# Optimization experiments

Hardware: AMD Instinct MI355X
Metric: run time of the kernel (lower is better)

## Reference

```python
import jax, jax.numpy as jnp
import numpy as np

B, N, E = 16, 64, 512
C_IMG = 512
H1, H2, H3 = 256, 128, 64
U, R = 8, 8
BBC = 9
EH1, EH2 = 64, 64
BBOX_POS_MAX = 1024.0
EPS = 1e-5


def setup_inputs():
    key = jax.random.key(0)
    ks = jax.random.split(key, 24)
    f = lambda i, shape, s=0.05: jax.random.normal(ks[i], shape, jnp.float32) * s
    return {
        'roi_features': f(0, (B, N, C_IMG), 1.0),
        'batch_bboxes': jax.random.uniform(ks[1], (B, N, 4)) * BBOX_POS_MAX,
        'batch_directions': jax.random.uniform(ks[2], (B, N, 4)),
        'batch_priorities': jax.random.uniform(ks[3], (B, N)),
        'w1': f(4, (C_IMG, H1)), 'b1': f(5, (H1,)),
        'bn1_g': jnp.ones((H1,)), 'bn1_b': jnp.zeros((H1,)),
        'bn1_m': jnp.zeros((H1,)), 'bn1_v': jnp.ones((H1,)),
        'w2': f(6, (H1, H2)), 'b2': f(7, (H2,)),
        'bn2_g': jnp.ones((H2,)), 'bn2_b': jnp.zeros((H2,)),
        'bn2_m': jnp.zeros((H2,)), 'bn2_v': jnp.ones((H2,)),
        'w3': f(8, (H2, H3)), 'b3': f(9, (H3,)),
        'wn': f(10, (H3, U)), 'bn_c': f(11, (U,)),
        'we1': f(12, (2 * BBC, EH1)), 'be1': f(13, (EH1,)),
        'we2': f(14, (EH1, EH2)), 'be2': f(15, (EH2,)),
        'wei': f(16, (EH2, R)), 'bei': f(17, (R,)),
        'edge_index': jax.random.randint(ks[18], (B, 2, E), 0, N, dtype=jnp.int32),
    }


def _bn(x, g, b, m, v):
    # BatchNorm1d in eval mode (running stats)
    return (x - m) * jax.lax.rsqrt(v + EPS) * g + b


def _build_see(edge_index):
    # Padded neighbor table replacing edge_index2dict:
    # see[b,n,0] = n, then srcs of edges with dst==n, in original edge order.
    src = edge_index[:, 0, :]                                   # [B,E]
    dst = edge_index[:, 1, :]                                   # [B,E]
    eq = dst[:, :, None] == dst[:, None, :]                     # [B,E,E]
    lower = jnp.tril(jnp.ones((E, E), bool), -1)
    pos = jnp.sum(eq & lower, axis=-1) + 1                      # rank within dst group, +1 for self slot
    see = jnp.zeros((B, N, N), jnp.int32).at[:, :, 0].set(jnp.arange(N, dtype=jnp.int32))
    b_idx = jnp.arange(B)[:, None]
    see = see.at[b_idx, dst, pos].set(src, mode='drop')
    deg = jnp.zeros((B, N), jnp.int32).at[b_idx, dst].add(1)
    count = jnp.minimum(deg + 1, N)
    mask = (jnp.arange(N)[None, None, :] < count[:, :, None]).astype(jnp.float32)  # [B,N,N]
    return see, mask


def _forward(roi_features, batch_bboxes, batch_directions, batch_priorities,
             w1, b1, bn1_g, bn1_b, bn1_m, bn1_v,
             w2, b2, bn2_g, bn2_b, bn2_m, bn2_v,
             w3, b3, wn, bn_c,
             we1, be1, we2, be2, wei, bei, edge_index):
    see, mask = _build_see(edge_index)
    # --- node branch (node_predictor + node_concept_interpreter) ---
    x = roi_features.reshape(B * N, C_IMG)
    x = jax.nn.relu(_bn(x @ w1 + b1, bn1_g, bn1_b, bn1_m, bn1_v))
    x = jax.nn.relu(_bn(x @ w2 + b2, bn2_g, bn2_b, bn2_m, bn2_v))
    x = jax.nn.relu(x @ w3 + b3)
    node_c = jax.nn.sigmoid(x @ wn + bn_c).reshape(B, N, U)
    # get_nlm_unary_concepts: gather per-node neighborhood into dense [B,N,N,U]
    gu = jax.vmap(lambda u, s: u[s])(node_c, see)               # [B,N,N,U]
    node_concepts = (gu * mask[..., None]).reshape(B * N, N, U)
    # --- edge branch ---
    attr = jnp.concatenate([batch_bboxes / BBOX_POS_MAX, batch_directions,
                            batch_priorities[..., None]], axis=-1)  # [B,N,BBC]
    pair = jnp.concatenate([
        jnp.broadcast_to(attr[:, :, None, :], (B, N, N, BBC)),
        jnp.broadcast_to(attr[:, None, :, :], (B, N, N, BBC))], axis=-1).reshape(-1, 2 * BBC)
    e = jax.nn.relu(pair @ we1 + be1)
    e = jax.nn.relu(e @ we2 + be2)
    rel = jax.nn.sigmoid(e @ wei + bei).reshape(B, N, N, R)
    # get_nlm_binary_concepts: rel[b, see[b,n,i], see[b,n,j]] with zero padding
    def per_b(r, s, m):
        g = r[s[:, :, None], s[:, None, :]]                     # [N,N,N,R]
        return g * (m[:, :, None, None] * m[:, None, :, None])
    edge_concepts = jax.vmap(per_b)(rel, see, mask).reshape(B * N, N, N, R)
    return node_concepts, edge_concepts


def reference(roi_features, batch_bboxes, batch_directions, batch_priorities,
              w1, b1, bn1_g, bn1_b, bn1_m, bn1_v,
              w2, b2, bn2_g, bn2_b, bn2_m, bn2_v,
              w3, b3, wn, bn_c,
              we1, be1, we2, be2, wei, bei, edge_index):
    return _forward(roi_features, batch_bboxes, batch_directions, batch_priorities,
                    w1, b1, bn1_g, bn1_b, bn1_m, bn1_v,
                    w2, b2, bn2_g, bn2_b, bn2_m, bn2_v,
                    w3, b3, wn, bn_c,
                    we1, be1, we2, be2, wei, bei, edge_index)
```

## Files before the change

kernel.cpp:

```cpp
#include <hip/hip_runtime.h>
#include <math.h>

#define BB    16
#define NN    64
#define EE    512
#define CIMG  512
#define H1D   256
#define H2D   128
#define H3D   64
#define UD    8
#define RD    8
#define BBCD  9
#define EH1D  64
#define EH2D  64
#define EPSF  1e-5f

typedef float nfloat4 __attribute__((ext_vector_type(4)));

__global__ __launch_bounds__(256) void fused1_kernel(
    const int* __restrict__ edge_index,
    const float* __restrict__ bboxes,
    const float* __restrict__ dirs,
    const float* __restrict__ prios,
    const float* __restrict__ we1,
    const float* __restrict__ be1,
    int* __restrict__ see, int* __restrict__ cnt,
    float* __restrict__ P, float* __restrict__ Q,
    const float* __restrict__ roi,
    const float* __restrict__ w1, const float* __restrict__ b1,
    const float* __restrict__ g1, const float* __restrict__ bt1,
    const float* __restrict__ m1, const float* __restrict__ v1,
    const float* __restrict__ w2, const float* __restrict__ b2,
    const float* __restrict__ g2, const float* __restrict__ bt2,
    const float* __restrict__ m2, const float* __restrict__ v2,
    const float* __restrict__ w3, const float* __restrict__ b3,
    const float* __restrict__ wn, const float* __restrict__ bnc,
    float* __restrict__ node_c,
    float* __restrict__ out_edge)
{
    __shared__ union {
        struct {
            int src[EE];
            int dst[EE];
            int see[NN * NN];
            float attr[NN][BBCD];
        } p;
        struct {
            float part[4096];
            float h1[4][H1D];
            float h2[4][H2D];
            float h3[4][H3D];
        } n;
    } sm;

    const int t = threadIdx.x;

    if (blockIdx.x >= BB + 256) {
        const int id = blockIdx.x - (BB + 256);
        nfloat4* dst = (nfloat4*)(out_edge + (size_t)id * NN * NN * RD);
        const nfloat4 z = {0.f, 0.f, 0.f, 0.f};
        #pragma unroll
        for (int it = 0; it < 16; ++it) {
            int task = it * 256 + t;
            __builtin_nontemporal_store(z, dst + task * 2);
            __builtin_nontemporal_store(z, dst + task * 2 + 1);
        }
        return;
    }

    if (blockIdx.x < BB) {
        const int b = blockIdx.x;
        const int* ei = edge_index + b * 2 * EE;
        for (int e = t; e < EE; e += 256) {
            sm.p.src[e] = ei[e];
            sm.p.dst[e] = ei[EE + e];
        }
        for (int x = t; x < NN * NN; x += 256)
            sm.p.see[x] = ((x & (NN - 1)) == 0) ? (x >> 6) : 0;
        if (t < NN) {
            const float* bbp = bboxes + (b * NN + t) * 4;
            const float* ddp = dirs + (b * NN + t) * 4;
            sm.p.attr[t][0] = bbp[0] * (1.0f / 1024.0f);
            sm.p.attr[t][1] = bbp[1] * (1.0f / 1024.0f);
            sm.p.attr[t][2] = bbp[2] * (1.0f / 1024.0f);
            sm.p.attr[t][3] = bbp[3] * (1.0f / 1024.0f);
            sm.p.attr[t][4] = ddp[0];
            sm.p.attr[t][5] = ddp[1];
            sm.p.attr[t][6] = ddp[2];
            sm.p.attr[t][7] = ddp[3];
            sm.p.attr[t][8] = prios[b * NN + t];
        }
        __syncthreads();

        if (t < NN) {
            int pos = 0;
            #pragma unroll 8
            for (int e = 0; e < EE; ++e) {
                if (sm.p.dst[e] == t) {
                    ++pos;
                    if (pos < NN) sm.p.see[t * NN + pos] = sm.p.src[e];
                }
            }
            int c = pos + 1;
            cnt[b * NN + t] = (c < NN) ? c : NN;
        }
        __syncthreads();

        {
            int4* dst4 = (int4*)(see + b * NN * NN);
            const int4* src4 = (const int4*)sm.p.see;
            for (int x = t; x < (NN * NN) / 4; x += 256) dst4[x] = src4[x];
        }

        for (int x = t; x < NN * EH1D; x += 256) {
            int n = x >> 6, o = x & 63;
            float p = 0.f;
            float q = be1[o];
            #pragma unroll
            for (int c = 0; c < BBCD; ++c) {
                float a = sm.p.attr[n][c];
                p = fmaf(a, we1[c * EH1D + o], p);
                q = fmaf(a, we1[(BBCD + c) * EH1D + o], q);
            }
            P[(b * NN + n) * EH1D + o] = p;
            Q[(b * NN + n) * EH1D + o] = q;
        }
        return;
    }

    const int row0 = (blockIdx.x - BB) * 4;
    float* part = sm.n.part;

    {
        const int og = t & 63, kg = t >> 6;
        const float4* w1v = (const float4*)w1;
        const float4* roiv = (const float4*)(roi + (size_t)row0 * CIMG);
        float acc[4][4];
        #pragma unroll
        for (int r = 0; r < 4; ++r)
            #pragma unroll
            for (int c = 0; c < 4; ++c) acc[r][c] = 0.f;

        for (int cq = 0; cq < 32; ++cq) {
            const int c4 = kg * 32 + cq;
            float x[4][4], w[4][4];
            #pragma unroll
            for (int r = 0; r < 4; ++r) {
                float4 v = roiv[r * 128 + c4];
                x[r][0] = v.x; x[r][1] = v.y; x[r][2] = v.z; x[r][3] = v.w;
            }
            #pragma unroll
            for (int q = 0; q < 4; ++q) {
                float4 v = w1v[(size_t)(c4 * 4 + q) * 64 + og];
                w[q][0] = v.x; w[q][1] = v.y; w[q][2] = v.z; w[q][3] = v.w;
            }
            #pragma unroll
            for (int r = 0; r < 4; ++r)
                #pragma unroll
                for (int q = 0; q < 4; ++q)
                    #pragma unroll
                    for (int c = 0; c < 4; ++c)
                        acc[r][c] = fmaf(x[r][q], w[q][c], acc[r][c]);
        }
        #pragma unroll
        for (int r = 0; r < 4; ++r) {
            float4 v = {acc[r][0], acc[r][1], acc[r][2], acc[r][3]};
            *(float4*)(part + (kg * 4 + r) * 256 + og * 4) = v;
        }
    }
    __syncthreads();
    {
        const int o = t;
        const float bias = b1[o];
        const float scale = rsqrtf(v1[o] + EPSF) * g1[o];
        const float beta = bt1[o];
        const float mu = m1[o];
        #pragma unroll
        for (int r = 0; r < 4; ++r) {
            float s = part[(0 * 4 + r) * 256 + o] + part[(1 * 4 + r) * 256 + o]
                    + part[(2 * 4 + r) * 256 + o] + part[(3 * 4 + r) * 256 + o];
            sm.n.h1[r][o] = fmaxf(0.f, (s + bias - mu) * scale + beta);
        }
    }
    __syncthreads();

    {
        const int og = t & 31, kg = t >> 5;
        const float4* w2v = (const float4*)w2;
        float acc[4][4];
        #pragma unroll
        for (int r = 0; r < 4; ++r)
            #pragma unroll
            for (int c = 0; c < 4; ++c) acc[r][c] = 0.f;

        #pragma unroll
        for (int cq = 0; cq < 8; ++cq) {
            const int c4 = kg * 8 + cq;
            float x[4][4], w[4][4];
            #pragma unroll
            for (int r = 0; r < 4; ++r) {
                float4 v = *(const float4*)&sm.n.h1[r][c4 * 4];
                x[r][0] = v.x; x[r][1] = v.y; x[r][2] = v.z; x[r][3] = v.w;
            }
            #pragma unroll
            for (int q = 0; q < 4; ++q) {
                float4 v = w2v[(size_t)(c4 * 4 + q) * 32 + og];
                w[q][0] = v.x; w[q][1] = v.y; w[q][2] = v.z; w[q][3] = v.w;
            }
            #pragma unroll
            for (int r = 0; r < 4; ++r)
                #pragma unroll
                for (int q = 0; q < 4; ++q)
                    #pragma unroll
                    for (int c = 0; c < 4; ++c)
                        acc[r][c] = fmaf(x[r][q], w[q][c], acc[r][c]);
        }
        #pragma unroll
        for (int r = 0; r < 4; ++r) {
            float4 v = {acc[r][0], acc[r][1], acc[r][2], acc[r][3]};
            *(float4*)(part + (kg * 4 + r) * 128 + og * 4) = v;
        }
    }
    __syncthreads();
    {
        const int o = t & 127;
        const int rp = t >> 7;
        const float bias = b2[o];
        const float scale = rsqrtf(v2[o] + EPSF) * g2[o];
        const float beta = bt2[o];
        const float mu = m2[o];
        #pragma unroll
        for (int rr = 0; rr < 2; ++rr) {
            const int r = rp + rr * 2;
            float s = 0.f;
            #pragma unroll
            for (int kg = 0; kg < 8; ++kg) s += part[(kg * 4 + r) * 128 + o];
            sm.n.h2[r][o] = fmaxf(0.f, (s + bias - mu) * scale + beta);
        }
    }
    __syncthreads();

    {
        const int og = t & 15, kg = t >> 4;
        const float4* w3v = (const float4*)w3;
        float acc[4][4];
        #pragma unroll
        for (int r = 0; r < 4; ++r)
            #pragma unroll
            for (int c = 0; c < 4; ++c) acc[r][c] = 0.f;

        #pragma unroll
        for (int cq = 0; cq < 2; ++cq) {
            const int c4 = kg * 2 + cq;
            float x[4][4], w[4][4];
            #pragma unroll
            for (int r = 0; r < 4; ++r) {
                float4 v = *(const float4*)&sm.n.h2[r][c4 * 4];
                x[r][0] = v.x; x[r][1] = v.y; x[r][2] = v.z; x[r][3] = v.w;
            }
            #pragma unroll
            for (int q = 0; q < 4; ++q) {
                float4 v = w3v[(size_t)(c4 * 4 + q) * 16 + og];
                w[q][0] = v.x; w[q][1] = v.y; w[q][2] = v.z; w[q][3] = v.w;
            }
            #pragma unroll
            for (int r = 0; r < 4; ++r)
                #pragma unroll
                for (int q = 0; q < 4; ++q)
                    #pragma unroll
                    for (int c = 0; c < 4; ++c)
                        acc[r][c] = fmaf(x[r][q], w[q][c], acc[r][c]);
        }
        #pragma unroll
        for (int r = 0; r < 4; ++r) {
            float4 v = {acc[r][0], acc[r][1], acc[r][2], acc[r][3]};
            *(float4*)(part + (kg * 4 + r) * 64 + og * 4) = v;
        }
    }
    __syncthreads();
    {
        const int o = t & 63;
        const int r = t >> 6;
        float s = b3[o];
        #pragma unroll
        for (int kg = 0; kg < 16; ++kg) s += part[(kg * 4 + r) * 64 + o];
        sm.n.h3[r][o] = fmaxf(0.f, s);
    }
    __syncthreads();

    if (t < 32) {
        const int o = t & 7, r = t >> 3;
        float a = bnc[o];
        #pragma unroll 8
        for (int c = 0; c < H3D; ++c) a = fmaf(sm.n.h3[r][c], wn[c * UD + o], a);
        node_c[(size_t)(row0 + r) * UD + o] = 1.f / (1.f + expf(-a));
    }
}

__global__ __launch_bounds__(256) void edge_mlp_kernel(
    const float* __restrict__ P, const float* __restrict__ Q,
    const float* __restrict__ we2, const float* __restrict__ be2,
    const float* __restrict__ wei, const float* __restrict__ bei,
    float* __restrict__ rel)
{
    __shared__ float e1_s[NN * 68];
    __shared__ float qw_s[NN * EH1D];
    __shared__ float wei_s[EH2D * RD];
    __shared__ float Pi_s[EH1D];
    __shared__ float be2_s[EH2D];
    __shared__ float bei_s[RD];

    const int t = threadIdx.x;
    const int b = blockIdx.x >> 6;
    const int i = blockIdx.x & 63;

    {
        const float4* Qb4 = (const float4*)(Q + (size_t)b * NN * EH1D);
        float4* qw4 = (float4*)qw_s;
        #pragma unroll
        for (int x = 0; x < 4; ++x) qw4[x * 256 + t] = Qb4[x * 256 + t];
        if (t < EH1D) Pi_s[t] = P[(size_t)(b * NN + i) * EH1D + t];
        if (t < 128) ((float4*)wei_s)[t] = ((const float4*)wei)[t];
        if (t < EH2D) be2_s[t] = be2[t];
        if (t < RD) bei_s[t] = bei[t];
    }
    __syncthreads();

    {
        const int j = t & 63, cg = t >> 6;
        const float4* qrow = (const float4*)(qw_s + j * EH1D);
        const float4* prow = (const float4*)Pi_s;
        #pragma unroll
        for (int q = 0; q < 4; ++q) {
            int c4 = cg * 4 + q;
            float4 qv = qrow[c4];
            float4 pv = prow[c4];
            float4 ev;
            ev.x = fmaxf(0.f, qv.x + pv.x);
            ev.y = fmaxf(0.f, qv.y + pv.y);
            ev.z = fmaxf(0.f, qv.z + pv.z);
            ev.w = fmaxf(0.f, qv.w + pv.w);
            *(float4*)(e1_s + j * 68 + c4 * 4) = ev;
        }
    }
    __syncthreads();

    {
        const float4* w4 = (const float4*)we2;
        float4* qw4 = (float4*)qw_s;
        #pragma unroll
        for (int x = 0; x < 4; ++x) qw4[x * 256 + t] = w4[x * 256 + t];
    }
    __syncthreads();

    const int tx = t & 15, ty = t >> 4;
    const int o0 = tx * 4, j0 = ty * 4;
    float acc[4][4];
    #pragma unroll
    for (int r = 0; r < 4; ++r)
        #pragma unroll
        for (int o = 0; o < 4; ++o) acc[r][o] = 0.f;

    #pragma unroll 4
    for (int cg = 0; cg < 16; ++cg) {
        float ev[4][4];
        #pragma unroll
        for (int r = 0; r < 4; ++r) {
            float4 v = *(const float4*)(e1_s + (j0 + r) * 68 + cg * 4);
            ev[r][0] = v.x; ev[r][1] = v.y; ev[r][2] = v.z; ev[r][3] = v.w;
        }
        #pragma unroll
        for (int q = 0; q < 4; ++q) {
            float4 wv = *(const float4*)(qw_s + (cg * 4 + q) * EH1D + o0);
            #pragma unroll
            for (int r = 0; r < 4; ++r) {
                acc[r][0] = fmaf(ev[r][q], wv.x, acc[r][0]);
                acc[r][1] = fmaf(ev[r][q], wv.y, acc[r][1]);
                acc[r][2] = fmaf(ev[r][q], wv.z, acc[r][2]);
                acc[r][3] = fmaf(ev[r][q], wv.w, acc[r][3]);
            }
        }
    }

    {
        float4 bv = *(const float4*)(be2_s + o0);
        #pragma unroll
        for (int r = 0; r < 4; ++r) {
            float4 v;
            v.x = fmaxf(0.f, acc[r][0] + bv.x);
            v.y = fmaxf(0.f, acc[r][1] + bv.y);
            v.z = fmaxf(0.f, acc[r][2] + bv.z);
            v.w = fmaxf(0.f, acc[r][3] + bv.w);
            *(float4*)(e1_s + (j0 + r) * 68 + o0) = v;
        }
    }
    __syncthreads();

    {
        const int j = t >> 2;
        const int r0 = (t & 3) * 2;
        float a0 = bei_s[r0], a1 = bei_s[r0 + 1];
        const float* e2row = e1_s + j * 68;
        #pragma unroll
        for (int og = 0; og < 16; ++og) {
            float4 e2v = *(const float4*)(e2row + og * 4);
            float2 w0 = *(const float2*)(wei_s + (og * 4 + 0) * RD + r0);
            float2 w1 = *(const float2*)(wei_s + (og * 4 + 1) * RD + r0);
            float2 w2 = *(const float2*)(wei_s + (og * 4 + 2) * RD + r0);
            float2 w3 = *(const float2*)(wei_s + (og * 4 + 3) * RD + r0);
            a0 = fmaf(e2v.x, w0.x, a0); a1 = fmaf(e2v.x, w0.y, a1);
            a0 = fmaf(e2v.y, w1.x, a0); a1 = fmaf(e2v.y, w1.y, a1);
            a0 = fmaf(e2v.z, w2.x, a0); a1 = fmaf(e2v.z, w2.y, a1);
            a0 = fmaf(e2v.w, w3.x, a0); a1 = fmaf(e2v.w, w3.y, a1);
        }
        float2 o;
        o.x = 1.f / (1.f + expf(-a0));
        o.y = 1.f / (1.f + expf(-a1));
        *(float2*)(rel + ((size_t)(b * NN + i) * NN + j) * RD + r0) = o;
    }
}

__global__ __launch_bounds__(256) void gather_kernel(
    const int* __restrict__ see, const int* __restrict__ cnt,
    const float* __restrict__ node_c, const float* __restrict__ rel,
    float* __restrict__ out_node, float* __restrict__ out_edge)
{
    __shared__ int s_s[NN];

    const int t = threadIdx.x;
    const int bi = blockIdx.x;
    const int b = bi >> 6;
    const int c = cnt[bi];

    if (t < NN) s_s[t] = see[bi * NN + t];
    __syncthreads();

    if (t < NN) {
        const float m = (t < c) ? 1.f : 0.f;
        const float4* src = (const float4*)(node_c + (size_t)(b * NN + s_s[t]) * UD);
        float4 v0 = src[0], v1 = src[1];
        v0.x *= m; v0.y *= m; v0.z *= m; v0.w *= m;
        v1.x *= m; v1.y *= m; v1.z *= m; v1.w *= m;
        float4* dst = (float4*)(out_node + ((size_t)bi * NN + t) * UD);
        dst[0] = v0;
        dst[1] = v1;
    }

    const float* relb = rel + (size_t)b * NN * NN * RD;
    float* outb = out_edge + (size_t)bi * NN * NN * RD;

    const int total = c * c;
    for (int task = t; task < total; task += 256) {
        int j = task / c;
        int k = task - j * c;
        const float4* src =
            (const float4*)(relb + (size_t)(s_s[j] * NN + s_s[k]) * RD);
        float4 v0 = src[0], v1 = src[1];
        float4* dst = (float4*)(outb + ((size_t)j * NN + k) * RD);
        dst[0] = v0;
        dst[1] = v1;
    }
}

extern "C" void kernel_launch(void* const* d_in, const int* in_sizes, int n_in,
                              void* d_out, int out_size, void* d_ws, size_t ws_size,
                              hipStream_t stream)
{
    const float* roi  = (const float*)d_in[0];
    const float* bbox = (const float*)d_in[1];
    const float* dirs = (const float*)d_in[2];
    const float* prio = (const float*)d_in[3];
    const float* w1   = (const float*)d_in[4];
    const float* b1   = (const float*)d_in[5];
    const float* g1   = (const float*)d_in[6];
    const float* bt1  = (const float*)d_in[7];
    const float* m1   = (const float*)d_in[8];
    const float* v1   = (const float*)d_in[9];
    const float* w2   = (const float*)d_in[10];
    const float* b2   = (const float*)d_in[11];
    const float* g2   = (const float*)d_in[12];
    const float* bt2  = (const float*)d_in[13];
    const float* m2   = (const float*)d_in[14];
    const float* v2   = (const float*)d_in[15];
    const float* w3   = (const float*)d_in[16];
    const float* b3   = (const float*)d_in[17];
    const float* wn   = (const float*)d_in[18];
    const float* bnc  = (const float*)d_in[19];
    const float* we1  = (const float*)d_in[20];
    const float* be1  = (const float*)d_in[21];
    const float* we2  = (const float*)d_in[22];
    const float* be2  = (const float*)d_in[23];
    const float* wei  = (const float*)d_in[24];
    const float* bei  = (const float*)d_in[25];
    const int* edge_index = (const int*)d_in[26];

    char* ws = (char*)d_ws;
    int*   see    = (int*)ws;   ws += (size_t)BB * NN * NN * 4;
    int*   cnt    = (int*)ws;   ws += (size_t)BB * NN * 4;
    float* Pbuf   = (float*)ws; ws += (size_t)BB * NN * EH1D * 4;
    float* Qbuf   = (float*)ws; ws += (size_t)BB * NN * EH1D * 4;
    float* node_c = (float*)ws; ws += (size_t)BB * NN * UD * 4;
    float* rel    = (float*)ws; ws += (size_t)BB * NN * NN * RD * 4;

    float* out_node = (float*)d_out;
    float* out_edge = (float*)d_out + (size_t)BB * NN * NN * UD;

    hipLaunchKernelGGL(fused1_kernel, dim3(BB + 256 + BB * NN), dim3(256), 0, stream,
                       edge_index, bbox, dirs, prio, we1, be1,
                       see, cnt, Pbuf, Qbuf,
                       roi, w1, b1, g1, bt1, m1, v1,
                       w2, b2, g2, bt2, m2, v2,
                       w3, b3, wn, bnc, node_c, out_edge);
    hipLaunchKernelGGL(edge_mlp_kernel, dim3(BB * NN), dim3(256), 0, stream,
                       Pbuf, Qbuf, we2, be2, wei, bei, rel);
    hipLaunchKernelGGL(gather_kernel, dim3(BB * NN), dim3(256), 0, stream,
                       see, cnt, node_c, rel, out_node, out_edge);
}
```

Before: 250.6 us.

## Fuse edge MLP into first kernel by recomputing first edge layer per block

The edge MLP kernel is folded into the first fused kernel as 1024 extra blocks. Each block recomputes the first edge layer (P and Q projections) from the box attributes instead of reading P/Q from a workspace, which removes one kernel launch, the P/Q global round trip and the dependency on the neighbor-table blocks. The cost is redundant first-layer arithmetic in every block and a larger shared-memory union, which could lower occupancy for the whole fused kernel.

```diff
diff --git a/kernel.cpp b/kernel.cpp
--- a/kernel.cpp
+++ b/kernel.cpp
@@ -17,15 +17,13 @@
 
 typedef float nfloat4 __attribute__((ext_vector_type(4)));
 
-__global__ __launch_bounds__(256) void fused1_kernel(
+__global__ __launch_bounds__(256) void fusedA_kernel(
     const int* __restrict__ edge_index,
     const float* __restrict__ bboxes,
     const float* __restrict__ dirs,
     const float* __restrict__ prios,
-    const float* __restrict__ we1,
-    const float* __restrict__ be1,
+    const float* __restrict__ we1, const float* __restrict__ be1,
     int* __restrict__ see, int* __restrict__ cnt,
-    float* __restrict__ P, float* __restrict__ Q,
     const float* __restrict__ roi,
     const float* __restrict__ w1, const float* __restrict__ b1,
     const float* __restrict__ g1, const float* __restrict__ bt1,
@@ -36,6 +34,9 @@
     const float* __restrict__ w3, const float* __restrict__ b3,
     const float* __restrict__ wn, const float* __restrict__ bnc,
     float* __restrict__ node_c,
+    const float* __restrict__ we2, const float* __restrict__ be2,
+    const float* __restrict__ wei, const float* __restrict__ bei,
+    float* __restrict__ rel,
     float* __restrict__ out_edge)
 {
     __shared__ union {
@@ -43,7 +44,6 @@
             int src[EE];
             int dst[EE];
             int see[NN * NN];
-            float attr[NN][BBCD];
         } p;
         struct {
             float part[4096];
@@ -51,12 +51,22 @@
             float h2[4][H2D];
             float h3[4][H3D];
         } n;
+        struct {
+            float e1[NN * 68];
+            float qw[NN * EH1D];
+            float wei[EH2D * RD];
+            float attr[NN][BBCD];
+            float we1[2 * BBCD * EH1D];
+            float Pi[EH1D];
+            float be2[EH2D];
+            float bei[RD];
+        } e;
     } sm;
 
     const int t = threadIdx.x;
 
-    if (blockIdx.x >= BB + 256) {
-        const int id = blockIdx.x - (BB + 256);
+    if (blockIdx.x >= BB + 256 + BB * NN) {
+        const int id = blockIdx.x - (BB + 256 + BB * NN);
         nfloat4* dst = (nfloat4*)(out_edge + (size_t)id * NN * NN * RD);
         const nfloat4 z = {0.f, 0.f, 0.f, 0.f};
         #pragma unroll
@@ -77,19 +87,6 @@
         }
         for (int x = t; x < NN * NN; x += 256)
             sm.p.see[x] = ((x & (NN - 1)) == 0) ? (x >> 6) : 0;
-        if (t < NN) {
-            const float* bbp = bboxes + (b * NN + t) * 4;
-            const float* ddp = dirs + (b * NN + t) * 4;
-            sm.p.attr[t][0] = bbp[0] * (1.0f / 1024.0f);
-            sm.p.attr[t][1] = bbp[1] * (1.0f / 1024.0f);
-            sm.p.attr[t][2] = bbp[2] * (1.0f / 1024.0f);
-            sm.p.attr[t][3] = bbp[3] * (1.0f / 1024.0f);
-            sm.p.attr[t][4] = ddp[0];
-            sm.p.attr[t][5] = ddp[1];
-            sm.p.attr[t][6] = ddp[2];
-            sm.p.attr[t][7] = ddp[3];
-            sm.p.attr[t][8] = prios[b * NN + t];
-        }
         __syncthreads();
 
         if (t < NN) {
@@ -106,24 +103,130 @@
         }
         __syncthreads();
 
+        int4* dst4 = (int4*)(see + b * NN * NN);
+        const int4* src4 = (const int4*)sm.p.see;
+        for (int x = t; x < (NN * NN) / 4; x += 256) dst4[x] = src4[x];
+        return;
+    }
+
+    if (blockIdx.x >= BB + 256) {
+        const int id = blockIdx.x - (BB + 256);
+        const int b = id >> 6;
+        const int i = id & 63;
+
+        if (t < NN) {
+            const float* bbp = bboxes + (b * NN + t) * 4;
+            const float* ddp = dirs + (b * NN + t) * 4;
+            sm.e.attr[t][0] = bbp[0] * (1.0f / 1024.0f);
+            sm.e.attr[t][1] = bbp[1] * (1.0f / 1024.0f);
+            sm.e.attr[t][2] = bbp[2] * (1.0f / 1024.0f);
+            sm.e.attr[t][3] = bbp[3] * (1.0f / 1024.0f);
+            sm.e.attr[t][4] = ddp[0];
+            sm.e.attr[t][5] = ddp[1];
+            sm.e.attr[t][6] = ddp[2];
+            sm.e.attr[t][7] = ddp[3];
+            sm.e.attr[t][8] = prios[b * NN + t];
+        }
+        for (int x = t; x < 2 * BBCD * EH1D; x += 256) sm.e.we1[x] = we1[x];
         {
-            int4* dst4 = (int4*)(see + b * NN * NN);
-            const int4* src4 = (const int4*)sm.p.see;
-            for (int x = t; x < (NN * NN) / 4; x += 256) dst4[x] = src4[x];
-        }
-
-        for (int x = t; x < NN * EH1D; x += 256) {
-            int n = x >> 6, o = x & 63;
-            float p = 0.f;
-            float q = be1[o];
-            #pragma unroll
-            for (int c = 0; c < BBCD; ++c) {
-                float a = sm.p.attr[n][c];
-                p = fmaf(a, we1[c * EH1D + o], p);
-                q = fmaf(a, we1[(BBCD + c) * EH1D + o], q);
-            }
-            P[(b * NN + n) * EH1D + o] = p;
-            Q[(b * NN + n) * EH1D + o] = q;
+            const float4* w4 = (const float4*)we2;
+            float4* qw4 = (float4*)sm.e.qw;
+            #pragma unroll
+            for (int x = 0; x < 4; ++x) qw4[x * 256 + t] = w4[x * 256 + t];
+        }
+        if (t < 128) ((float4*)sm.e.wei)[t] = ((const float4*)wei)[t];
+        if (t < EH2D) sm.e.be2[t] = be2[t];
+        if (t < RD) sm.e.bei[t] = bei[t];
+        __syncthreads();
+
+        if (t < EH1D) {
+            float p = be1[t];
+            #pragma unroll
+            for (int c = 0; c < BBCD; ++c)
+                p = fmaf(sm.e.attr[i][c], sm.e.we1[c * EH1D + t], p);
+            sm.e.Pi[t] = p;
+        }
+        __syncthreads();
+
+        {
+            const int o = t & 63;
+            const int jw = t >> 6;
+            #pragma unroll
+            for (int jg = 0; jg < 16; ++jg) {
+                const int j = jg * 4 + jw;
+                float a = sm.e.Pi[o];
+                #pragma unroll
+                for (int c = 0; c < BBCD; ++c)
+                    a = fmaf(sm.e.attr[j][c], sm.e.we1[(BBCD + c) * EH1D + o], a);
+                sm.e.e1[j * 68 + o] = fmaxf(0.f, a);
+            }
+        }
+        __syncthreads();
+
+        const int tx = t & 15, ty = t >> 4;
+        const int o0 = tx * 4, j0 = ty * 4;
+        float acc[4][4];
+        #pragma unroll
+        for (int r = 0; r < 4; ++r)
+            #pragma unroll
+            for (int o = 0; o < 4; ++o) acc[r][o] = 0.f;
+
+        #pragma unroll 4
+        for (int cg = 0; cg < 16; ++cg) {
+            float ev[4][4];
+            #pragma unroll
+            for (int r = 0; r < 4; ++r) {
+                float4 v = *(const float4*)(sm.e.e1 + (j0 + r) * 68 + cg * 4);
+                ev[r][0] = v.x; ev[r][1] = v.y; ev[r][2] = v.z; ev[r][3] = v.w;
+            }
+            #pragma unroll
+            for (int q = 0; q < 4; ++q) {
+                float4 wv = *(const float4*)(sm.e.qw + (cg * 4 + q) * EH1D + o0);
+                #pragma unroll
+                for (int r = 0; r < 4; ++r) {
+                    acc[r][0] = fmaf(ev[r][q], wv.x, acc[r][0]);
+                    acc[r][1] = fmaf(ev[r][q], wv.y, acc[r][1]);
+                    acc[r][2] = fmaf(ev[r][q], wv.z, acc[r][2]);
+                    acc[r][3] = fmaf(ev[r][q], wv.w, acc[r][3]);
+                }
+            }
+        }
+
+        {
+            float4 bv = *(const float4*)(sm.e.be2 + o0);
+            #pragma unroll
+            for (int r = 0; r < 4; ++r) {
+                float4 v;
+                v.x = fmaxf(0.f, acc[r][0] + bv.x);
+                v.y = fmaxf(0.f, acc[r][1] + bv.y);
+                v.z = fmaxf(0.f, acc[r][2] + bv.z);
+                v.w = fmaxf(0.f, acc[r][3] + bv.w);
+                *(float4*)(sm.e.e1 + (j0 + r) * 68 + o0) = v;
+            }
+        }
+        __syncthreads();
+
+        {
+            const int j = t >> 2;
+            const int r0 = (t & 3) * 2;
+            float a0 = sm.e.bei[r0], a1 = sm.e.bei[r0 + 1];
+            const float* e2row = sm.e.e1 + j * 68;
+            #pragma unroll
+            for (int og = 0; og < 16; ++og) {
+                float4 e2v = *(const float4*)(e2row + og * 4);
+                float2 w0 = *(const float2*)(sm.e.wei + (og * 4 + 0) * RD + r0);
+                float2 w1 = *(const float2*)(sm.e.wei + (og * 4 + 1) * RD + r0);
+                float2 w2 = *(const float2*)(sm.e.wei + (og * 4 + 2) * RD + r0);
+                float2 w3 = *(const float2*)(sm.e.wei + (og * 4 + 3) * RD + r0);
+                a0 = fmaf(e2v.x, w0.x, a0); a1 = fmaf(e2v.x, w0.y, a1);
+                a0 = fmaf(e2v.y, w1.x, a0); a1 = fmaf(e2v.y, w1.y, a1);
+                a0 = fmaf(e2v.z, w2.x, a0); a1 = fmaf(e2v.z, w2.y, a1);
+                a0 = fmaf(e2v.w, w3.x, a0); a1 = fmaf(e2v.w, w3.y, a1);
+            }
+            float2 o;
+            o.x = 1.f / (1.f + expf(-a0));
+            o.y = 1.f / (1.f + expf(-a1));
+            *(float2*)(rel + ((size_t)id * NN + j) * RD + r0) = o;
         }
         return;
     }
@@ -294,129 +397,6 @@
         #pragma unroll 8
         for (int c = 0; c < H3D; ++c) a = fmaf(sm.n.h3[r][c], wn[c * UD + o], a);
         node_c[(size_t)(row0 + r) * UD + o] = 1.f / (1.f + expf(-a));
-    }
-}
-
-__global__ __launch_bounds__(256) void edge_mlp_kernel(
-    const float* __restrict__ P, const float* __restrict__ Q,
-    const float* __restrict__ we2, const float* __restrict__ be2,
-    const float* __restrict__ wei, const float* __restrict__ bei,
-    float* __restrict__ rel)
-{
-    __shared__ float e1_s[NN * 68];
-    __shared__ float qw_s[NN * EH1D];
-    __shared__ float wei_s[EH2D * RD];
-    __shared__ float Pi_s[EH1D];
-    __shared__ float be2_s[EH2D];
-    __shared__ float bei_s[RD];
-
-    const int t = threadIdx.x;
-    const int b = blockIdx.x >> 6;
-    const int i = blockIdx.x & 63;
-
-    {
-        const float4* Qb4 = (const float4*)(Q + (size_t)b * NN * EH1D);
-        float4* qw4 = (float4*)qw_s;
-        #pragma unroll
-        for (int x = 0; x < 4; ++x) qw4[x * 256 + t] = Qb4[x * 256 + t];
-        if (t < EH1D) Pi_s[t] = P[(size_t)(b * NN + i) * EH1D + t];
-        if (t < 128) ((float4*)wei_s)[t] = ((const float4*)wei)[t];
-        if (t < EH2D) be2_s[t] = be2[t];
-        if (t < RD) bei_s[t] = bei[t];
-    }
-    __syncthreads();
-
-    {
-        const int j = t & 63, cg = t >> 6;
-        const float4* qrow = (const float4*)(qw_s + j * EH1D);
-        const float4* prow = (const float4*)Pi_s;
-        #pragma unroll
-        for (int q = 0; q < 4; ++q) {
-            int c4 = cg * 4 + q;
-            float4 qv = qrow[c4];
-            float4 pv = prow[c4];
-            float4 ev;
-            ev.x = fmaxf(0.f, qv.x + pv.x);
-            ev.y = fmaxf(0.f, qv.y + pv.y);
-            ev.z = fmaxf(0.f, qv.z + pv.z);
-            ev.w = fmaxf(0.f, qv.w + pv.w);
-            *(float4*)(e1_s + j * 68 + c4 * 4) = ev;
-        }
-    }
-    __syncthreads();
-
-    {
-        const float4* w4 = (const float4*)we2;
-        float4* qw4 = (float4*)qw_s;
-        #pragma unroll
-        for (int x = 0; x < 4; ++x) qw4[x * 256 + t] = w4[x * 256 + t];
-    }
-    __syncthreads();
-
-    const int tx = t & 15, ty = t >> 4;
-    const int o0 = tx * 4, j0 = ty * 4;
-    float acc[4][4];
-    #pragma unroll
-    for (int r = 0; r < 4; ++r)
-        #pragma unroll
-        for (int o = 0; o < 4; ++o) acc[r][o] = 0.f;
-
-    #pragma unroll 4
-    for (int cg = 0; cg < 16; ++cg) {
-        float ev[4][4];
-        #pragma unroll
-        for (int r = 0; r < 4; ++r) {
-            float4 v = *(const float4*)(e1_s + (j0 + r) * 68 + cg * 4);
-            ev[r][0] = v.x; ev[r][1] = v.y; ev[r][2] = v.z; ev[r][3] = v.w;
-        }
-        #pragma unroll
-        for (int q = 0; q < 4; ++q) {
-            float4 wv = *(const float4*)(qw_s + (cg * 4 + q) * EH1D + o0);
-            #pragma unroll
-            for (int r = 0; r < 4; ++r) {
-                acc[r][0] = fmaf(ev[r][q], wv.x, acc[r][0]);
-                acc[r][1] = fmaf(ev[r][q], wv.y, acc[r][1]);
-                acc[r][2] = fmaf(ev[r][q], wv.z, acc[r][2]);
-                acc[r][3] = fmaf(ev[r][q], wv.w, acc[r][3]);
-            }
-        }
-    }
-
-    {
-        float4 bv = *(const float4*)(be2_s + o0);
-        #pragma unroll
-        for (int r = 0; r < 4; ++r) {
-            float4 v;
-            v.x = fmaxf(0.f, acc[r][0] + bv.x);
-            v.y = fmaxf(0.f, acc[r][1] + bv.y);
-            v.z = fmaxf(0.f, acc[r][2] + bv.z);
-            v.w = fmaxf(0.f, acc[r][3] + bv.w);
-            *(float4*)(e1_s + (j0 + r) * 68 + o0) = v;
-        }
-    }
-    __syncthreads();
-
-    {
-        const int j = t >> 2;
-        const int r0 = (t & 3) * 2;
-        float a0 = bei_s[r0], a1 = bei_s[r0 + 1];
-        const float* e2row = e1_s + j * 68;
-        #pragma unroll
-        for (int og = 0; og < 16; ++og) {
-            float4 e2v = *(const float4*)(e2row + og * 4);
-            float2 w0 = *(const float2*)(wei_s + (og * 4 + 0) * RD + r0);
-            float2 w1 = *(const float2*)(wei_s + (og * 4 + 1) * RD + r0);
-            float2 w2 = *(const float2*)(wei_s + (og * 4 + 2) * RD + r0);
-            float2 w3 = *(const float2*)(wei_s + (og * 4 + 3) * RD + r0);
-            a0 = fmaf(e2v.x, w0.x, a0); a1 = fmaf(e2v.x, w0.y, a1);
-            a0 = fmaf(e2v.y, w1.x, a0); a1 = fmaf(e2v.y, w1.y, a1);
-            a0 = fmaf(e2v.z, w2.x, a0); a1 = fmaf(e2v.z, w2.y, a1);
-            a0 = fmaf(e2v.w, w3.x, a0); a1 = fmaf(e2v.w, w3.y, a1);
-        }
-        float2 o;
-        o.x = 1.f / (1.f + expf(-a0));
-        o.y = 1.f / (1.f + expf(-a1));
-        *(float2*)(rel + ((size_t)(b * NN + i) * NN + j) * RD + r0) = o;
     }
 }
 
@@ -497,22 +477,20 @@
     char* ws = (char*)d_ws;
     int*   see    = (int*)ws;   ws += (size_t)BB * NN * NN * 4;
     int*   cnt    = (int*)ws;   ws += (size_t)BB * NN * 4;
-    float* Pbuf   = (float*)ws; ws += (size_t)BB * NN * EH1D * 4;
-    float* Qbuf   = (float*)ws; ws += (size_t)BB * NN * EH1D * 4;
     float* node_c = (float*)ws; ws += (size_t)BB * NN * UD * 4;
     float* rel    = (float*)ws; ws += (size_t)BB * NN * NN * RD * 4;
 
     float* out_node = (float*)d_out;
     float* out_edge = (float*)d_out + (size_t)BB * NN * NN * UD;
 
-    hipLaunchKernelGGL(fused1_kernel, dim3(BB + 256 + BB * NN), dim3(256), 0, stream,
+    hipLaunchKernelGGL(fusedA_kernel,
+                       dim3(BB + 256 + BB * NN + BB * NN), dim3(256), 0, stream,
                        edge_index, bbox, dirs, prio, we1, be1,
-                       see, cnt, Pbuf, Qbuf,
+                       see, cnt,
                        roi, w1, b1, g1, bt1, m1, v1,
                        w2, b2, g2, bt2, m2, v2,
-                       w3, b3, wn, bnc, node_c, out_edge);
-    hipLaunchKernelGGL(edge_mlp_kernel, dim3(BB * NN), dim3(256), 0, stream,
-                       Pbuf, Qbuf, we2, be2, wei, bei, rel);
+                       w3, b3, wn, bnc, node_c,
+                       we2, be2, wei, bei, rel, out_edge);
     hipLaunchKernelGGL(gather_kernel, dim3(BB * NN), dim3(256), 0, stream,
                        see, cnt, node_c, rel, out_node, out_edge);
 }
```

Result: slower. 261.2 us (+4.2%).
